# Kernel tuning notes

Hardware: AMD Instinct MI355X
Metric: run time of the kernel (lower is better)

## Reference

```python
import jax, jax.numpy as jnp
import numpy as np

TEMP = 0.05
EPS_SUM = 1e-6
EPS_LOG = 1e-6

B, D, M, C = 512, 256, 131072, 2000


def setup_inputs() -> dict:
    key = jax.random.key(0)
    k1, k2, k3, k4 = jax.random.split(key, 4)
    results = jax.random.normal(k1, (B, D), dtype=jnp.float32)
    indexes = jax.random.randint(k2, (B,), 0, M, dtype=jnp.int64)
    # memory bank is L2-normalized in practice (_update_feature normalizes)
    feats = jax.random.normal(k3, (M, D), dtype=jnp.float32)
    feats = feats / jnp.maximum(jnp.linalg.norm(feats, axis=1, keepdims=True), 1e-12)
    labels = jax.random.randint(k4, (M,), 0, C, dtype=jnp.int64)
    return {"results": results, "indexes": indexes, "features": feats,
            "labels": labels, "num_clusters": C}


def reference(results, indexes, features, labels, num_clusters):
    # L2 normalize inputs (F.normalize, p=2, dim=1)
    inputs = results / jnp.maximum(jnp.linalg.norm(results, axis=1, keepdims=True), 1e-12)
    # HM forward: similarity against memory bank, scaled by temperature
    sims = jnp.einsum('bd,md->bm', inputs, features) / TEMP  # [B, M]
    # segment-sum over memory slots grouped by cluster label (index_add_)
    sim_c = jax.ops.segment_sum(sims.T, labels, num_segments=num_clusters)  # [C, B]
    counts = jax.ops.segment_sum(jnp.ones((features.shape[0],), dtype=sims.dtype),
                                 labels, num_segments=num_clusters)  # [C]
    mask = counts > 0  # [C]
    denom = jnp.where(mask, counts, 1.0)[:, None]
    vec = (sim_c / denom).T  # [B, C] cluster-averaged similarities
    # masked softmax over clusters (matches original: exp then mask then normalize)
    exps = jnp.exp(vec) * mask[None, :].astype(vec.dtype)
    probs = exps / (jnp.sum(exps, axis=1, keepdims=True) + EPS_SUM)
    # NLL loss with targets = labels[indexes]
    targets = labels[indexes]  # [B]
    logp = jnp.log(probs + EPS_LOG)
    picked = jnp.take_along_axis(logp, targets[:, None], axis=1)[:, 0]
    return -jnp.mean(picked)
```

## Files before the change

kernel.cpp:

```cpp
#include <hip/hip_runtime.h>
#include <hip/hip_bf16.h>

#define TEMP_F   0.05f
#define B_       512
#define D_       256
#define M_       131072
#define C_       2000
#define CAP      256

typedef __attribute__((ext_vector_type(8))) short bf16x8;
typedef __attribute__((ext_vector_type(4))) float f32x4;

__device__ __forceinline__ unsigned short f2bf(float x) {
    __hip_bfloat16 h = __float2bfloat16(x);
    return *reinterpret_cast<unsigned short*>(&h);
}

__device__ __forceinline__ float block_reduce_sum256(float v, float* smem) {
    #pragma unroll
    for (int off = 32; off >= 1; off >>= 1) v += __shfl_xor(v, off, 64);
    int wave = threadIdx.x >> 6;
    if ((threadIdx.x & 63) == 0) smem[wave] = v;
    __syncthreads();
    return smem[0] + smem[1] + smem[2] + smem[3];
}

__global__ __launch_bounds__(256) void prep_kernel(
        const float* __restrict__ results, unsigned short* __restrict__ inp,
        int* __restrict__ cursor, float* __restrict__ out) {
    __shared__ float smem[4];
    int b = blockIdx.x;
    if (b < B_) {
        float v = results[b * D_ + threadIdx.x];
        float s = block_reduce_sum256(v * v, smem);
        float inv = 1.0f / fmaxf(sqrtf(s), 1e-12f);
        inp[b * D_ + threadIdx.x] = f2bf(v * inv);
    } else {
        int i = (b - B_) * 256 + threadIdx.x;
        if (i < C_) cursor[i] = 0;
        if (i == 0) out[0] = 0.0f;
    }
}

__global__ __launch_bounds__(256) void scatter_kernel(
        const int* __restrict__ labels, int* __restrict__ cursor,
        int* __restrict__ member) {
    int m = blockIdx.x * 256 + threadIdx.x;
    int c = labels[m];
    int pos = atomicAdd(&cursor[c], 1);
    if (pos < CAP) member[c * CAP + pos] = m;
}

__global__ __launch_bounds__(256) void centroid_kernel(
        const float* __restrict__ features, const int* __restrict__ cursor,
        const int* __restrict__ member, unsigned short* __restrict__ cs) {
    __shared__ int mlist[CAP];
    int c = blockIdx.x, t = threadIdx.x;
    int n = cursor[c];
    int nn = min(n, CAP);
    if (t < nn) mlist[t] = member[c * CAP + t];
    __syncthreads();
    float a0 = 0.f, a1 = 0.f, a2 = 0.f, a3 = 0.f;
    int i = 0;
    for (; i + 4 <= nn; i += 4) {
        a0 += features[(size_t)mlist[i + 0] * D_ + t];
        a1 += features[(size_t)mlist[i + 1] * D_ + t];
        a2 += features[(size_t)mlist[i + 2] * D_ + t];
        a3 += features[(size_t)mlist[i + 3] * D_ + t];
    }
    for (; i < nn; ++i) a0 += features[(size_t)mlist[i] * D_ + t];
    float acc = (a0 + a1) + (a2 + a3);
    float scale = 1.0f / (TEMP_F * (float)max(n, 1));
    cs[c * D_ + t] = f2bf(acc * scale);
}

__global__ __launch_bounds__(256) void gemm_kernel(
        const unsigned short* __restrict__ inp, const unsigned short* __restrict__ cs,
        float* __restrict__ vec) {
    int wave = threadIdx.x >> 6;
    int lane = threadIdx.x & 63;
    int tile = blockIdx.x * 4 + wave;
    int tb = tile / 125;
    int tc = tile - tb * 125;
    int row = lane & 15;
    int kg  = lane >> 4;
    const unsigned short* ap = inp + (size_t)(tb * 16 + row) * D_ + kg * 8;
    const unsigned short* bp = cs  + (size_t)(tc * 16 + row) * D_ + kg * 8;
    f32x4 acc = {0.f, 0.f, 0.f, 0.f};
    #pragma unroll
    for (int k0 = 0; k0 < D_; k0 += 32) {
        bf16x8 a = *reinterpret_cast<const bf16x8*>(ap + k0);
        bf16x8 b = *reinterpret_cast<const bf16x8*>(bp + k0);
        acc = __builtin_amdgcn_mfma_f32_16x16x32_bf16(a, b, acc, 0, 0, 0);
    }
    int ccol  = tc * 16 + (lane & 15);
    int brow0 = tb * 16 + kg * 4;
    #pragma unroll
    for (int r = 0; r < 4; ++r)
        vec[(size_t)(brow0 + r) * C_ + ccol] = acc[r];
}

__global__ __launch_bounds__(256) void loss_kernel(
        const float* __restrict__ vec, const int* __restrict__ cursor,
        const int* __restrict__ labels, const int* __restrict__ indexes,
        float* __restrict__ out) {
    __shared__ float smem[4];
    int b = blockIdx.x, t = threadIdx.x;
    float s = 0.f;
    for (int c = t; c < C_; c += 256) {
        float v = vec[(size_t)b * C_ + c];
        s += (cursor[c] > 0) ? expf(v) : 0.f;
    }
    float S = block_reduce_sum256(s, smem);
    if (t == 0) {
        int tgt = labels[indexes[b]];
        float pt = expf(vec[(size_t)b * C_ + tgt]) / (S + 1e-6f);
        atomicAdd(out, -logf(pt + 1e-6f) * (1.0f / (float)B_));
    }
}

extern "C" void kernel_launch(void* const* d_in, const int* in_sizes, int n_in,
                              void* d_out, int out_size, void* d_ws, size_t ws_size,
                              hipStream_t stream) {
    const float* results  = (const float*)d_in[0];
    const int*   indexes  = (const int*)d_in[1];
    const float* features = (const float*)d_in[2];
    const int*   labels   = (const int*)d_in[3];
    float* out = (float*)d_out;

    char* w = (char*)d_ws;
    unsigned short* inp  = (unsigned short*)(w);
    int*            curs = (int*)(w + 262144);
    int*            memb = (int*)(w + 262144 + 8192);
    unsigned short* cs   = (unsigned short*)(w + 262144 + 8192 + 2097152);
    float*          vec  = (float*)(w + 262144 + 8192 + 2097152 + 1048576);

    prep_kernel<<<B_ + (C_ + 255) / 256, 256, 0, stream>>>(results, inp, curs, out);
    scatter_kernel<<<M_ / 256, 256, 0, stream>>>(labels, curs, memb);
    centroid_kernel<<<C_, 256, 0, stream>>>(features, curs, memb, cs);
    gemm_kernel<<<1000, 256, 0, stream>>>(inp, cs, vec);
    loss_kernel<<<B_, 256, 0, stream>>>(vec, curs, labels, indexes, out);
}
```

Before: 245.3 us.

## Fold input normalization into loss, fuse cast into scatter, vectorize centroid gather

```diff
diff --git a/kernel.cpp b/kernel.cpp
--- a/kernel.cpp
+++ b/kernel.cpp
@@ -10,6 +10,7 @@
 
 typedef __attribute__((ext_vector_type(8))) short bf16x8;
 typedef __attribute__((ext_vector_type(4))) float f32x4;
+typedef __attribute__((ext_vector_type(4))) unsigned short u16x4;
 
 __device__ __forceinline__ unsigned short f2bf(float x) {
     __hip_bfloat16 h = __float2bfloat16(x);
@@ -17,6 +18,7 @@
 }
 
 __device__ __forceinline__ float block_reduce_sum256(float v, float* smem) {
+    __syncthreads();
     #pragma unroll
     for (int off = 32; off >= 1; off >>= 1) v += __shfl_xor(v, off, 64);
     int wave = threadIdx.x >> 6;
@@ -25,53 +27,52 @@
     return smem[0] + smem[1] + smem[2] + smem[3];
 }
 
-__global__ __launch_bounds__(256) void prep_kernel(
-        const float* __restrict__ results, unsigned short* __restrict__ inp,
-        int* __restrict__ cursor, float* __restrict__ out) {
-    __shared__ float smem[4];
-    int b = blockIdx.x;
-    if (b < B_) {
-        float v = results[b * D_ + threadIdx.x];
-        float s = block_reduce_sum256(v * v, smem);
-        float inv = 1.0f / fmaxf(sqrtf(s), 1e-12f);
-        inp[b * D_ + threadIdx.x] = f2bf(v * inv);
-    } else {
-        int i = (b - B_) * 256 + threadIdx.x;
-        if (i < C_) cursor[i] = 0;
-        if (i == 0) out[0] = 0.0f;
-    }
-}
-
-__global__ __launch_bounds__(256) void scatter_kernel(
+__global__ __launch_bounds__(256) void scatter_cast_kernel(
         const int* __restrict__ labels, int* __restrict__ cursor,
-        int* __restrict__ member) {
-    int m = blockIdx.x * 256 + threadIdx.x;
+        int* __restrict__ member,
+        const float* __restrict__ results, unsigned short* __restrict__ inp) {
+    int t = threadIdx.x, blk = blockIdx.x;
+    int m = blk * 256 + t;
     int c = labels[m];
     int pos = atomicAdd(&cursor[c], 1);
     if (pos < CAP) member[c * CAP + pos] = m;
+    inp[blk * 256 + t] = f2bf(results[blk * 256 + t]);
 }
 
 __global__ __launch_bounds__(256) void centroid_kernel(
         const float* __restrict__ features, const int* __restrict__ cursor,
         const int* __restrict__ member, unsigned short* __restrict__ cs) {
     __shared__ int mlist[CAP];
+    __shared__ f32x4 part[4][64];
     int c = blockIdx.x, t = threadIdx.x;
     int n = cursor[c];
     int nn = min(n, CAP);
     if (t < nn) mlist[t] = member[c * CAP + t];
     __syncthreads();
-    float a0 = 0.f, a1 = 0.f, a2 = 0.f, a3 = 0.f;
-    int i = 0;
-    for (; i + 4 <= nn; i += 4) {
-        a0 += features[(size_t)mlist[i + 0] * D_ + t];
-        a1 += features[(size_t)mlist[i + 1] * D_ + t];
-        a2 += features[(size_t)mlist[i + 2] * D_ + t];
-        a3 += features[(size_t)mlist[i + 3] * D_ + t];
+    int w = t >> 6;
+    int l = t & 63;
+    f32x4 a0 = {0.f, 0.f, 0.f, 0.f}, a1 = {0.f, 0.f, 0.f, 0.f};
+    int i = w;
+    for (; i + 4 < nn; i += 8) {
+        f32x4 v0 = *reinterpret_cast<const f32x4*>(&features[(size_t)mlist[i] * D_ + l * 4]);
+        f32x4 v1 = *reinterpret_cast<const f32x4*>(&features[(size_t)mlist[i + 4] * D_ + l * 4]);
+        a0 += v0;
+        a1 += v1;
     }
-    for (; i < nn; ++i) a0 += features[(size_t)mlist[i] * D_ + t];
-    float acc = (a0 + a1) + (a2 + a3);
-    float scale = 1.0f / (TEMP_F * (float)max(n, 1));
-    cs[c * D_ + t] = f2bf(acc * scale);
+    if (i < nn)
+        a0 += *reinterpret_cast<const f32x4*>(&features[(size_t)mlist[i] * D_ + l * 4]);
+    part[w][l] = a0 + a1;
+    __syncthreads();
+    if (t < 64) {
+        f32x4 s = part[0][t] + part[1][t] + part[2][t] + part[3][t];
+        float scale = 1.0f / (TEMP_F * (float)max(n, 1));
+        u16x4 o;
+        o[0] = f2bf(s[0] * scale);
+        o[1] = f2bf(s[1] * scale);
+        o[2] = f2bf(s[2] * scale);
+        o[3] = f2bf(s[3] * scale);
+        *reinterpret_cast<u16x4*>(&cs[c * D_ + t * 4]) = o;
+    }
 }
 
 __global__ __launch_bounds__(256) void gemm_kernel(
@@ -101,20 +102,23 @@
 }
 
 __global__ __launch_bounds__(256) void loss_kernel(
-        const float* __restrict__ vec, const int* __restrict__ cursor,
-        const int* __restrict__ labels, const int* __restrict__ indexes,
-        float* __restrict__ out) {
+        const float* __restrict__ results, const float* __restrict__ vec,
+        const int* __restrict__ cursor, const int* __restrict__ labels,
+        const int* __restrict__ indexes, float* __restrict__ out) {
     __shared__ float smem[4];
     int b = blockIdx.x, t = threadIdx.x;
+    float rv = results[b * D_ + t];
+    float nrm2 = block_reduce_sum256(rv * rv, smem);
+    float inv = 1.0f / fmaxf(sqrtf(nrm2), 1e-12f);
     float s = 0.f;
     for (int c = t; c < C_; c += 256) {
-        float v = vec[(size_t)b * C_ + c];
+        float v = vec[(size_t)b * C_ + c] * inv;
         s += (cursor[c] > 0) ? expf(v) : 0.f;
     }
     float S = block_reduce_sum256(s, smem);
     if (t == 0) {
         int tgt = labels[indexes[b]];
-        float pt = expf(vec[(size_t)b * C_ + tgt]) / (S + 1e-6f);
+        float pt = expf(vec[(size_t)b * C_ + tgt] * inv) / (S + 1e-6f);
         atomicAdd(out, -logf(pt + 1e-6f) * (1.0f / (float)B_));
     }
 }
@@ -135,9 +139,10 @@
     unsigned short* cs   = (unsigned short*)(w + 262144 + 8192 + 2097152);
     float*          vec  = (float*)(w + 262144 + 8192 + 2097152 + 1048576);
 
-    prep_kernel<<<B_ + (C_ + 255) / 256, 256, 0, stream>>>(results, inp, curs, out);
-    scatter_kernel<<<M_ / 256, 256, 0, stream>>>(labels, curs, memb);
+    hipMemsetAsync(curs, 0, C_ * sizeof(int), stream);
+    hipMemsetAsync(out, 0, sizeof(float), stream);
+    scatter_cast_kernel<<<M_ / 256, 256, 0, stream>>>(labels, curs, memb, results, inp);
     centroid_kernel<<<C_, 256, 0, stream>>>(features, curs, memb, cs);
     gemm_kernel<<<1000, 256, 0, stream>>>(inp, cs, vec);
-    loss_kernel<<<B_, 256, 0, stream>>>(vec, curs, labels, indexes, out);
+    loss_kernel<<<B_, 256, 0, stream>>>(results, vec, curs, labels, indexes, out);
 }
```

New measurement: 248.3 us. Within noise of the previous version (+1.2%).
